# Kernel tuning notes

Hardware: AMD Instinct MI355X
Metric: run time of the kernel (lower is better)

The kernel has to match this reference:

```python
import jax, jax.numpy as jnp
import numpy as np

B, S, D, H, KD, HID = 8, 1024, 512, 8, 64, 32


def setup_inputs() -> dict:
    key = jax.random.key(0)
    ks = jax.random.split(key, 13)
    s = 0.05
    return {
        "src": jax.random.normal(ks[0], (B, S, D), jnp.float32),
        "Wq": jax.random.normal(ks[1], (H, KD, D), jnp.float32) * s,
        "Wk": jax.random.normal(ks[2], (H, KD, D), jnp.float32) * s,
        "Wv": jax.random.normal(ks[3], (H, KD, D), jnp.float32) * s,
        "c_raw": jnp.ones((H,), jnp.float32),              # nn.Parameter(1.0) per head
        "L": jnp.full((H,), 2.0, jnp.float32),             # nn.Parameter(2.0) per head
        "w1": jax.random.normal(ks[4], (H, HID), jnp.float32) * s,   # Linear(1,HID) weight
        "b1": jax.random.normal(ks[5], (H, HID), jnp.float32) * s,
        "W2": jax.random.normal(ks[6], (H, HID, HID), jnp.float32) * s,  # [out,in]
        "b2": jax.random.normal(ks[7], (H, HID), jnp.float32) * s,
        "w3": jax.random.normal(ks[8], (H, HID), jnp.float32) * s,   # Linear(HID,1) weight
        "b3": jax.random.normal(ks[9], (H,), jnp.float32) * s,
        "Wo": jax.random.normal(ks[10], (D, D), jnp.float32) * s,
    }


def _gelu(x):
    return jax.nn.gelu(x, approximate=False)  # torch nn.GELU default (erf)


def reference(src, Wq, Wk, Wv, c_raw, L, w1, b1, W2, b2, w3, b3, Wo):
    Bc, Sc, Dc = src.shape
    Hh, Kd = Wq.shape[0], Wq.shape[1]
    # ---- FIRE bias: raw[i,j] = log1p(c*(i-j)) / log1p(c*max(L, i+1)) for j<i else 0
    ii = jnp.arange(Sc, dtype=jnp.float32)[:, None]   # [S,1]
    jj = jnp.arange(Sc, dtype=jnp.float32)[None, :]   # [1,S]
    d = ii - jj                                       # [S,S]
    c = jax.nn.softplus(c_raw)[:, None, None]         # [H,1,1]
    num = jnp.log1p(c * jnp.where(d > 0, d, 1.0)[None])          # safe for d<=0
    den = jnp.log1p(c * jnp.maximum(L[:, None, None], ii[None] + 1.0))
    raw = jnp.where(d[None] > 0, num / den, 0.0)      # [H,S,S]
    # ---- f_theta MLP applied elementwise (Linear(1,h)->GELU->Linear(h,h)->GELU->Linear(h,1))
    h1 = _gelu(raw[..., None] * w1[:, None, None, :] + b1[:, None, None, :])   # [H,S,S,HID]
    h2 = _gelu(jnp.einsum('hijk,hlk->hijl', h1, W2) + b2[:, None, None, :])    # [H,S,S,HID]
    bias = jnp.einsum('hijk,hk->hij', h2, w3) + b3[:, None, None]              # [H,S,S]
    # ---- causal mask (strict upper triangle -> -inf)
    causal = jnp.arange(Sc)[None, :] > jnp.arange(Sc)[:, None]
    bias = jnp.where(causal[None], -jnp.inf, bias)
    # ---- attention per head
    q = jnp.einsum('bsd,hkd->bhsk', src, Wq)
    k = jnp.einsum('bsd,hkd->bhsk', src, Wk)
    v = jnp.einsum('bsd,hkd->bhsk', src, Wv)
    logits = jnp.einsum('bhik,bhjk->bhij', q, k) / jnp.sqrt(jnp.float32(Kd)) + bias[None]
    attn = jax.nn.softmax(logits, axis=-1)
    o = jnp.einsum('bhij,bhjk->bhik', attn, v)        # [B,H,S,KD]
    o = jnp.transpose(o, (0, 2, 1, 3)).reshape(Bc, Sc, Hh * Kd)  # concat heads
    return o @ Wo.T
```

## Files before the change

kernel.cpp:

```cpp
#include <hip/hip_runtime.h>
#include <math.h>

#define S_LEN 1024
#define NHEAD 8
#define BATCH 8
#define KDIM  64
#define HID   32
#define NT    2048
#define TRI(q) ((q) * ((q) + 1) / 2)
#define PERM(m) (((m) & 0x20) | (((m) & 0x0C) << 1) | (((m) & 0x10) >> 2) | ((m) & 3))
#define SWZ(row) (((((row) >> 3) & 1) << 2) | ((row) & 3))

typedef __attribute__((ext_vector_type(8))) short bf16x8;
typedef __attribute__((ext_vector_type(4))) float f32x4;
typedef unsigned short ushort_t;

__device__ inline ushort_t f2bf(float f) {
  union { float f; unsigned u; } v; v.f = f;
  unsigned u = v.u;
  return (ushort_t)((u + 0x7FFFu + ((u >> 16) & 1u)) >> 16);
}
__device__ inline float bf2f(ushort_t u) {
  union { unsigned x; float f; } v; v.x = ((unsigned)u) << 16; return v.f;
}

__device__ inline void gl_lds16(const ushort_t* g, ushort_t* l) {
  __builtin_amdgcn_global_load_lds(
      (const __attribute__((address_space(1))) unsigned int*)g,
      (__attribute__((address_space(3))) unsigned int*)l, 16, 0, 0);
}

__global__ __launch_bounds__(256) void prep(
    const float* __restrict__ s, const float* __restrict__ wq,
    const float* __restrict__ wk, const float* __restrict__ wv,
    const float* __restrict__ wo,
    ushort_t* __restrict__ sb, ushort_t* __restrict__ wqb,
    ushort_t* __restrict__ wkb, ushort_t* __restrict__ wvb,
    ushort_t* __restrict__ wob,
    const float* __restrict__ c_raw, const float* __restrict__ Lp,
    const float* __restrict__ w1, const float* __restrict__ b1,
    const float* __restrict__ W2, const float* __restrict__ b2,
    const float* __restrict__ w3, const float* __restrict__ b3,
    float* __restrict__ num_g, float* __restrict__ rden_g,
    float* __restrict__ gtab_g) {
  __shared__ float h1s[8][33];
  const int bx = blockIdx.x;
  const int tid = threadIdx.x;
  if (bx < 5120) {
    const float* src; ushort_t* dst; int base; float scale = 1.0f;
    if (bx < 4096)      { src = s;  dst = sb;  base = bx; }
    else if (bx < 4352) { src = wq; dst = wqb; base = bx - 4096; scale = 0.125f; }
    else if (bx < 4608) { src = wk; dst = wkb; base = bx - 4352; }
    else if (bx < 4864) { src = wv; dst = wvb; base = bx - 4608; }
    else                { src = wo; dst = wob; base = bx - 4864; }
    const int i = (base * 256 + tid) * 4;
    float4 v = *(const float4*)&src[i];
    ushort4 o;
    o.x = f2bf(v.x * scale); o.y = f2bf(v.y * scale);
    o.z = f2bf(v.z * scale); o.w = f2bf(v.w * scale);
    *(ushort4*)&dst[i] = o;
  } else {
    const int idx = bx - 5120;
    const int h = idx / 257;
    const int xb = idx % 257;
    const float cr = c_raw[h];
    const float c = (cr > 20.f) ? cr : log1pf(expf(cr));
    const int gid = xb * 256 + tid;
    if (gid < S_LEN) {
      num_g[h * S_LEN + gid] = log1pf(c * (float)gid);
      rden_g[h * S_LEN + gid] = 1.0f / log1pf(c * fmaxf(Lp[h], (float)(gid + 1)));
    }
    const int pl = tid >> 5;
    const int j = tid & 31;
    const int pt = xb * 8 + pl;
    const float x = (float)pt * (1.0f / NT);
    float v = x * w1[h * HID + j] + b1[h * HID + j];
    h1s[pl][j] = 0.5f * v * (1.0f + erff(v * 0.70710678118f));
    __syncthreads();
    float sm = b2[h * HID + j];
    const float* w2r = W2 + ((size_t)(h * HID + j)) * HID;
    #pragma unroll
    for (int k = 0; k < HID; ++k) sm += w2r[k] * h1s[pl][k];
    float g = 0.5f * sm * (1.0f + erff(sm * 0.70710678118f));
    float y = w3[h * HID + j] * g;
    #pragma unroll
    for (int off = 1; off < 32; off <<= 1) y += __shfl_xor(y, off);
    if (j == 0 && pt <= NT) gtab_g[h * (NT + 1) + pt] = y + b3[h];
  }
}

__device__ __forceinline__ void gemm_tile(
    ushort_t* sAB, const ushort_t* __restrict__ A, const ushort_t* __restrict__ Wp,
    void* __restrict__ outp, int mode, int m0, int n0, int tid) {
  ushort_t* sA = sAB;
  ushort_t* sB = sAB + 8192;
  const int lane = tid & 63, w = tid >> 6, quad = lane >> 4, l16 = lane & 15;
  const int wr = w >> 1, wc = w & 1;
  f32x4 acc[4][4];
  #pragma unroll
  for (int ia = 0; ia < 4; ++ia)
    #pragma unroll
    for (int ib = 0; ib < 4; ++ib) acc[ia][ib] = (f32x4)0.0f;

  const int r8 = lane >> 3;
  const int gc = (lane & 7) ^ r8;
  const int sw = l16 & 7;

  for (int kt = 0; kt < 512; kt += 64) {
    __syncthreads();
    #pragma unroll
    for (int j = 0; j < 4; ++j) {
      const int row = j * 32 + w * 8 + r8;
      gl_lds16(&A[(size_t)(m0 + row) * 512 + kt + gc * 8], &sA[(j * 32 + w * 8) * 64]);
      gl_lds16(&Wp[(size_t)(n0 + row) * 512 + kt + gc * 8], &sB[(j * 32 + w * 8) * 64]);
    }
    __syncthreads();
    #pragma unroll
    for (int ks = 0; ks < 2; ++ks) {
      const int off = ((ks * 4 + quad) ^ sw) * 8;
      bf16x8 af[4], bfr[4];
      #pragma unroll
      for (int i = 0; i < 4; ++i) {
        af[i] = *(bf16x8*)&sA[(wr * 64 + i * 16 + l16) * 64 + off];
        bfr[i] = *(bf16x8*)&sB[(wc * 64 + i * 16 + l16) * 64 + off];
      }
      #pragma unroll
      for (int ia = 0; ia < 4; ++ia)
        #pragma unroll
        for (int ib = 0; ib < 4; ++ib)
          acc[ia][ib] = __builtin_amdgcn_mfma_f32_16x16x32_bf16(af[ia], bfr[ib], acc[ia][ib], 0, 0, 0);
    }
  }

  if (mode == 2) {
    __syncthreads();
    #pragma unroll
    for (int ia = 0; ia < 4; ++ia)
      #pragma unroll
      for (int ib = 0; ib < 4; ++ib)
        #pragma unroll
        for (int r = 0; r < 4; ++r) {
          int nl = wc * 64 + ib * 16 + l16;
          int ml = wr * 64 + ia * 16 + quad * 4 + r;
          sAB[nl * 128 + (((ml >> 3) ^ (nl & 7)) * 8) + (ml & 7)] = f2bf(acc[ia][ib][r]);
        }
    __syncthreads();
    const int nl = tid >> 1, halfm = tid & 1;
    const int ng = n0 + nl, hh = ng >> 6, kd = ng & 63;
    const int bb = m0 >> 10, sbase = m0 & 1023;
    ushort_t* vout = (ushort_t*)outp + (((size_t)(bb * NHEAD + hh)) * KDIM + kd) * S_LEN;
    #pragma unroll
    for (int c2 = 0; c2 < 8; ++c2) {
      int mc = halfm * 8 + c2;
      bf16x8 vr = *(bf16x8*)&sAB[nl * 128 + ((mc ^ (nl & 7)) * 8)];
      *(bf16x8*)&vout[sbase + mc * 8] = vr;
    }
    return;
  }
  #pragma unroll
  for (int ia = 0; ia < 4; ++ia) {
    #pragma unroll
    for (int ib = 0; ib < 4; ++ib) {
      #pragma unroll
      for (int r = 0; r < 4; ++r) {
        int m = m0 + wr * 64 + ia * 16 + quad * 4 + r;
        int n = n0 + wc * 64 + ib * 16 + l16;
        float v = acc[ia][ib][r];
        if (mode == 1) {
          int bb = m >> 10, ss = m & 1023, hh = n >> 6, kd = n & 63;
          ((ushort_t*)outp)[(((size_t)(bb * NHEAD + hh)) * S_LEN + ss) * KDIM + kd] = f2bf(v);
        } else {
          ((float*)outp)[(size_t)m * 512 + n] = v;
        }
      }
    }
  }
}

__global__ __launch_bounds__(256) void gemm_bias(
    const ushort_t* __restrict__ A,
    const ushort_t* __restrict__ W0, const ushort_t* __restrict__ W1,
    const ushort_t* __restrict__ W2w,
    void* __restrict__ out0, void* __restrict__ out1, void* __restrict__ out2,
    int scatter, int nGemm,
    const float* __restrict__ num_g, const float* __restrict__ rden_g,
    const float* __restrict__ gtab_g, ushort_t* __restrict__ biaspre) {
  __shared__ __align__(16) ushort_t sAB[16384];
  const int tid = threadIdx.x;
  if ((int)blockIdx.x < nGemm) {
    const int z = blockIdx.x >> 8;
    const int idx = blockIdx.x & 255;
    const int m0 = (idx & 63) * 128;
    const int n0 = (idx >> 6) * 128;
    const ushort_t* Wp = (z == 0) ? W0 : (z == 1) ? W1 : W2w;
    void* outp = (z == 0) ? out0 : (z == 1) ? out1 : out2;
    const int mode = scatter ? ((z == 2) ? 2 : 1) : 0;
    gemm_tile(sAB, A, Wp, outp, mode, m0, n0, tid);
  } else {
    const int idx = blockIdx.x - nGemm;
    const int h = idx / 68;
    const int pair = idx % 68;
    float* gtab_s = (float*)sAB;
    float* num_s = gtab_s + 2052;
    float* rden_s = num_s + 1024;
    for (int i = tid; i <= NT; i += 256) gtab_s[i] = gtab_g[h * (NT + 1) + i];
    for (int i = tid; i < S_LEN; i += 256) num_s[i] = num_g[h * S_LEN + i];
    const int sub = tid >> 7, tid2 = tid & 127;
    const int tileIdx = pair * 2 + sub;
    int qt = 0;
    while (TRI(qt + 1) <= tileIdx) ++qt;
    const int t = tileIdx - TRI(qt);
    if (tid2 < 64) rden_s[sub * 64 + tid2] = rden_g[h * S_LEN + qt * 64 + tid2];
    __syncthreads();
    const int w = tid2 >> 6, lane = tid2 & 63, quad = lane >> 4, l16 = lane & 15;
    ushort_t vals[32];
    #pragma unroll
    for (int qg = 0; qg < 2; ++qg) {
      const int iloc = w * 32 + qg * 16 + l16;
      const int i = qt * 64 + iloc;
      const float rden = rden_s[sub * 64 + iloc];
      #pragma unroll
      for (int nb = 0; nb < 4; ++nb)
        #pragma unroll
        for (int r = 0; r < 4; ++r) {
          const int m = nb * 16 + quad * 4 + r;
          const int j = t * 64 + PERM(m);
          ushort_t out;
          if (j > i) {
            out = 0xFF80;
          } else {
            const int d = i - j;
            float x = num_s[d] * rden;
            float tf = x * (float)NT;
            int it = (int)tf; it = it < (NT - 1) ? it : (NT - 1);
            float fr = tf - (float)it;
            float ga = gtab_s[it];
            out = f2bf(ga + (gtab_s[it + 1] - ga) * fr);
          }
          vals[qg * 16 + nb * 4 + r] = out;
        }
    }
    ushort_t* dst = &biaspre[((size_t)(h * 136 + tileIdx) * 128 + tid2) * 32];
    uint4 u[2];
    #pragma unroll
    for (int half = 0; half < 2; ++half) {
      #pragma unroll
      for (int v = 0; v < 8; ++v) ((ushort_t*)&u[0])[v] = vals[half * 16 + v];
      #pragma unroll
      for (int v = 0; v < 8; ++v) ((ushort_t*)&u[1])[v] = vals[half * 16 + 8 + v];
      *(uint4*)(dst + half * 16) = u[0];
      *(uint4*)(dst + half * 16 + 8) = u[1];
    }
  }
}

__global__ __launch_bounds__(128) void fire_attn_mfma(
    const ushort_t* __restrict__ Qg, const ushort_t* __restrict__ Kg,
    const ushort_t* __restrict__ Vtg, const ushort_t* __restrict__ biaspre,
    ushort_t* __restrict__ Ob) {
  __shared__ __align__(16) ushort_t Ks[64 * 64];
  __shared__ __align__(16) ushort_t Vt[64 * 64];
  const int tid = threadIdx.x;
  const int lane = tid & 63, w = tid >> 6, quad = lane >> 4, l16 = lane & 15;
  const int g = blockIdx.x >> 6;
  const int qt = (g < 8) ? (15 - g) : (g - 8);
  const int bh = blockIdx.x & 63, h = bh & 7, b = bh >> 3;

  bf16x8 q[2][2];
  {
    const size_t qb = (size_t)bh * S_LEN + qt * 64 + w * 32;
    #pragma unroll
    for (int qg = 0; qg < 2; ++qg)
      #pragma unroll
      for (int ks = 0; ks < 2; ++ks)
        q[qg][ks] = *(const bf16x8*)&Qg[(qb + qg * 16 + l16) * KDIM + ks * 32 + quad * 8];
  }

  const size_t kb = (size_t)bh * S_LEN * KDIM;
  const ushort_t* bptr = &biaspre[((size_t)(h * 136 + TRI(qt)) * 128 + tid) * 32];
  const int srow8 = lane >> 3;
  const int sc = lane & 7;

  f32x4 o[2][4];
  float ll[2] = {0.f, 0.f};
  #pragma unroll
  for (int qg = 0; qg < 2; ++qg)
    #pragma unroll
    for (int nb = 0; nb < 4; ++nb) o[qg][nb] = (f32x4)0.0f;

  for (int t = 0; t <= qt; ++t) {
    __syncthreads();
    #pragma unroll
    for (int j = 0; j < 4; ++j) {
      const int row = (w * 4 + j) * 8 + srow8;
      const int cc = sc ^ SWZ(row);
      gl_lds16(&Kg[kb + (size_t)(t * 64 + row) * 64 + cc * 8], &Ks[(w * 4 + j) * 512]);
      gl_lds16(&Vtg[kb + (size_t)row * 1024 + t * 64 + cc * 8], &Vt[(w * 4 + j) * 512]);
    }
    __syncthreads();

    uint4 bb0 = ((const uint4*)(bptr + (size_t)t * 4096))[0];
    uint4 bb1 = ((const uint4*)(bptr + (size_t)t * 4096))[1];
    uint4 bb2 = ((const uint4*)(bptr + (size_t)t * 4096))[2];
    uint4 bb3 = ((const uint4*)(bptr + (size_t)t * 4096))[3];

    f32x4 s[2][4];
    #pragma unroll
    for (int qg = 0; qg < 2; ++qg)
      #pragma unroll
      for (int nb = 0; nb < 4; ++nb) s[qg][nb] = (f32x4)0.0f;
    #pragma unroll
    for (int ks = 0; ks < 2; ++ks) {
      #pragma unroll
      for (int nb = 0; nb < 4; ++nb) {
        const int rk = PERM(nb * 16 + l16);
        bf16x8 ak = *(bf16x8*)&Ks[rk * 64 + (((ks * 4 + quad) ^ SWZ(rk)) * 8)];
        #pragma unroll
        for (int qg = 0; qg < 2; ++qg)
          s[qg][nb] = __builtin_amdgcn_mfma_f32_16x16x32_bf16(ak, q[qg][ks], s[qg][nb], 0, 0, 0);
      }
    }

    ushort_t eb[2][16];
    #pragma unroll
    for (int qg = 0; qg < 2; ++qg) {
      #pragma unroll
      for (int nb = 0; nb < 4; ++nb)
        #pragma unroll
        for (int r = 0; r < 4; ++r) {
          const int v = qg * 16 + nb * 4 + r;
          const uint4& bq = (v < 8) ? bb0 : (v < 16) ? bb1 : (v < 24) ? bb2 : bb3;
          ushort_t bu = ((const ushort_t*)&bq)[v & 7];
          float p = __expf(s[qg][nb][r] + bf2f(bu));
          ll[qg] += p;
          eb[qg][nb * 4 + r] = f2bf(p);
        }
    }

    #pragma unroll
    for (int ks = 0; ks < 2; ++ks) {
      bf16x8 pf[2];
      #pragma unroll
      for (int qg = 0; qg < 2; ++qg) {
        union { bf16x8 v; unsigned u[4]; } pk;
        pk.u[0] = (unsigned)eb[qg][(2 * ks) * 4 + 0] | ((unsigned)eb[qg][(2 * ks) * 4 + 1] << 16);
        pk.u[1] = (unsigned)eb[qg][(2 * ks) * 4 + 2] | ((unsigned)eb[qg][(2 * ks) * 4 + 3] << 16);
        pk.u[2] = (unsigned)eb[qg][(2 * ks + 1) * 4 + 0] | ((unsigned)eb[qg][(2 * ks + 1) * 4 + 1] << 16);
        pk.u[3] = (unsigned)eb[qg][(2 * ks + 1) * 4 + 2] | ((unsigned)eb[qg][(2 * ks + 1) * 4 + 3] << 16);
        pf[qg] = pk.v;
      }
      #pragma unroll
      for (int nb = 0; nb < 4; ++nb) {
        const int rv = nb * 16 + l16;
        bf16x8 av = *(bf16x8*)&Vt[rv * 64 + (((ks * 4 + quad) ^ SWZ(rv)) * 8)];
        #pragma unroll
        for (int qg = 0; qg < 2; ++qg)
          o[qg][nb] = __builtin_amdgcn_mfma_f32_16x16x32_bf16(av, pf[qg], o[qg][nb], 0, 0, 0);
      }
    }
  }

  #pragma unroll
  for (int qg = 0; qg < 2; ++qg) {
    float rs = ll[qg];
    rs += __shfl_xor(rs, 16);
    rs += __shfl_xor(rs, 32);
    const float rl = 1.0f / rs;
    const size_t ob = ((size_t)(b * S_LEN + qt * 64 + w * 32 + qg * 16 + l16)) * 512 + h * KDIM;
    #pragma unroll
    for (int nb = 0; nb < 4; ++nb) {
      ushort4 ov;
      ov.x = f2bf(o[qg][nb][0] * rl);
      ov.y = f2bf(o[qg][nb][1] * rl);
      ov.z = f2bf(o[qg][nb][2] * rl);
      ov.w = f2bf(o[qg][nb][3] * rl);
      *(ushort4*)&Ob[ob + nb * 16 + quad * 4] = ov;
    }
  }
}

extern "C" void kernel_launch(void* const* d_in, const int* in_sizes, int n_in,
                              void* d_out, int out_size, void* d_ws, size_t ws_size,
                              hipStream_t stream) {
  const float* src   = (const float*)d_in[0];
  const float* Wq    = (const float*)d_in[1];
  const float* Wk    = (const float*)d_in[2];
  const float* Wv    = (const float*)d_in[3];
  const float* c_raw = (const float*)d_in[4];
  const float* Lp    = (const float*)d_in[5];
  const float* w1    = (const float*)d_in[6];
  const float* b1    = (const float*)d_in[7];
  const float* W2    = (const float*)d_in[8];
  const float* b2    = (const float*)d_in[9];
  const float* w3    = (const float*)d_in[10];
  const float* b3    = (const float*)d_in[11];
  const float* Wo    = (const float*)d_in[12];
  float* outp = (float*)d_out;

  const size_t SRC_E = 4194304;
  const size_t W_E   = 262144;
  const size_t QKV_E = 4194304;
  ushort_t* srcb = (ushort_t*)d_ws;
  ushort_t* Wqb  = srcb + SRC_E;
  ushort_t* Wkb  = Wqb + W_E;
  ushort_t* Wvb  = Wkb + W_E;
  ushort_t* Wob  = Wvb + W_E;
  ushort_t* Qb   = Wob + W_E;
  ushort_t* Kb   = Qb + QKV_E;
  ushort_t* Vtb  = Kb + QKV_E;
  ushort_t* Obb  = Vtb + QKV_E;
  ushort_t* biaspre = Obb + QKV_E;
  float* numb  = (float*)(biaspre + (size_t)NHEAD * 136 * 128 * 32);
  float* rdenb = numb + NHEAD * S_LEN;
  float* gtabb = rdenb + NHEAD * S_LEN;

  hipLaunchKernelGGL(prep, dim3(7176), dim3(256), 0, stream,
                     src, Wq, Wk, Wv, Wo, srcb, Wqb, Wkb, Wvb, Wob,
                     c_raw, Lp, w1, b1, W2, b2, w3, b3, numb, rdenb, gtabb);
  hipLaunchKernelGGL(gemm_bias, dim3(1312), dim3(256), 0, stream,
                     srcb, Wqb, Wkb, Wvb, (void*)Qb, (void*)Kb, (void*)Vtb,
                     1, 768, numb, rdenb, gtabb, biaspre);
  hipLaunchKernelGGL(fire_attn_mfma, dim3(1024), dim3(128), 0, stream,
                     Qb, Kb, Vtb, biaspre, Obb);
  hipLaunchKernelGGL(gemm_bias, dim3(256), dim3(256), 0, stream,
                     Obb, Wob, Wob, Wob, (void*)outp, (void*)outp, (void*)outp,
                     0, 256, numb, rdenb, gtabb, biaspre);
}
```

Measured before the change: 170.9 us.

## Register-prefetch next K/V and GEMM tiles instead of direct global-to-LDS loads

Replaces the global_load_lds direct-to-LDS copies in both the projection GEMM and the attention loop with register-staged loads. The next tile is fetched into registers while the current tile is being computed, then written to swizzled LDS at the start of the next iteration. This is meant to hide global memory latency behind MFMA work. The cost is extra VGPRs and a separate LDS store pass, which could lower occupancy.

```diff
diff --git a/kernel.cpp b/kernel.cpp
--- a/kernel.cpp
+++ b/kernel.cpp
@@ -22,12 +22,6 @@
 }
 __device__ inline float bf2f(ushort_t u) {
   union { unsigned x; float f; } v; v.x = ((unsigned)u) << 16; return v.f;
-}
-
-__device__ inline void gl_lds16(const ushort_t* g, ushort_t* l) {
-  __builtin_amdgcn_global_load_lds(
-      (const __attribute__((address_space(1))) unsigned int*)g,
-      (__attribute__((address_space(3))) unsigned int*)l, 16, 0, 0);
 }
 
 __global__ __launch_bounds__(256) void prep(
@@ -102,19 +96,34 @@
     #pragma unroll
     for (int ib = 0; ib < 4; ++ib) acc[ia][ib] = (f32x4)0.0f;
 
-  const int r8 = lane >> 3;
-  const int gc = (lane & 7) ^ r8;
   const int sw = l16 & 7;
 
-  for (int kt = 0; kt < 512; kt += 64) {
-    __syncthreads();
-    #pragma unroll
-    for (int j = 0; j < 4; ++j) {
-      const int row = j * 32 + w * 8 + r8;
-      gl_lds16(&A[(size_t)(m0 + row) * 512 + kt + gc * 8], &sA[(j * 32 + w * 8) * 64]);
-      gl_lds16(&Wp[(size_t)(n0 + row) * 512 + kt + gc * 8], &sB[(j * 32 + w * 8) * 64]);
-    }
-    __syncthreads();
+  const int row = tid >> 1, half = tid & 1, r7 = row & 7;
+  const ushort_t* ag = &A[(size_t)(m0 + row) * 512 + half * 32];
+  const ushort_t* bg = &Wp[(size_t)(n0 + row) * 512 + half * 32];
+  uint4 pa[4], pb[4];
+  #pragma unroll
+  for (int i = 0; i < 4; ++i) {
+    pa[i] = *(const uint4*)(ag + i * 8);
+    pb[i] = *(const uint4*)(bg + i * 8);
+  }
+
+  for (int kt8 = 0; kt8 < 8; ++kt8) {
+    __syncthreads();
+    #pragma unroll
+    for (int i = 0; i < 4; ++i) {
+      const int c = half * 4 + i;
+      *(uint4*)&sA[row * 64 + ((c ^ r7) * 8)] = pa[i];
+      *(uint4*)&sB[row * 64 + ((c ^ r7) * 8)] = pb[i];
+    }
+    __syncthreads();
+    if (kt8 < 7) {
+      #pragma unroll
+      for (int i = 0; i < 4; ++i) {
+        pa[i] = *(const uint4*)(ag + (kt8 + 1) * 64 + i * 8);
+        pb[i] = *(const uint4*)(bg + (kt8 + 1) * 64 + i * 8);
+      }
+    }
     #pragma unroll
     for (int ks = 0; ks < 2; ++ks) {
       const int off = ((ks * 4 + quad) ^ sw) * 8;
@@ -278,8 +287,17 @@
 
   const size_t kb = (size_t)bh * S_LEN * KDIM;
   const ushort_t* bptr = &biaspre[((size_t)(h * 136 + TRI(qt)) * 128 + tid) * 32];
-  const int srow8 = lane >> 3;
-  const int sc = lane & 7;
+
+  const int srow = tid >> 1, shalf = tid & 1;
+  const int sswz = SWZ(srow);
+  const ushort_t* kg = &Kg[kb + (size_t)srow * 64 + shalf * 32];
+  const ushort_t* vg = &Vtg[kb + (size_t)srow * 1024 + shalf * 32];
+  uint4 pk[4], pv[4];
+  #pragma unroll
+  for (int i = 0; i < 4; ++i) {
+    pk[i] = *(const uint4*)(kg + i * 8);
+    pv[i] = *(const uint4*)(vg + i * 8);
+  }
 
   f32x4 o[2][4];
   float ll[2] = {0.f, 0.f};
@@ -291,13 +309,19 @@
   for (int t = 0; t <= qt; ++t) {
     __syncthreads();
     #pragma unroll
-    for (int j = 0; j < 4; ++j) {
-      const int row = (w * 4 + j) * 8 + srow8;
-      const int cc = sc ^ SWZ(row);
-      gl_lds16(&Kg[kb + (size_t)(t * 64 + row) * 64 + cc * 8], &Ks[(w * 4 + j) * 512]);
-      gl_lds16(&Vtg[kb + (size_t)row * 1024 + t * 64 + cc * 8], &Vt[(w * 4 + j) * 512]);
-    }
-    __syncthreads();
+    for (int i = 0; i < 4; ++i) {
+      const int c = shalf * 4 + i;
+      *(uint4*)&Ks[srow * 64 + ((c ^ sswz) * 8)] = pk[i];
+      *(uint4*)&Vt[srow * 64 + ((c ^ sswz) * 8)] = pv[i];
+    }
+    __syncthreads();
+    if (t < qt) {
+      #pragma unroll
+      for (int i = 0; i < 4; ++i) {
+        pk[i] = *(const uint4*)(kg + (size_t)(t + 1) * 4096 + i * 8);
+        pv[i] = *(const uint4*)(vg + (size_t)(t + 1) * 64 + i * 8);
+      }
+    }
 
     uint4 bb0 = ((const uint4*)(bptr + (size_t)t * 4096))[0];
     uint4 bb1 = ((const uint4*)(bptr + (size_t)t * 4096))[1];
@@ -342,12 +366,12 @@
       bf16x8 pf[2];
       #pragma unroll
       for (int qg = 0; qg < 2; ++qg) {
-        union { bf16x8 v; unsigned u[4]; } pk;
-        pk.u[0] = (unsigned)eb[qg][(2 * ks) * 4 + 0] | ((unsigned)eb[qg][(2 * ks) * 4 + 1] << 16);
-        pk.u[1] = (unsigned)eb[qg][(2 * ks) * 4 + 2] | ((unsigned)eb[qg][(2 * ks) * 4 + 3] << 16);
-        pk.u[2] = (unsigned)eb[qg][(2 * ks + 1) * 4 + 0] | ((unsigned)eb[qg][(2 * ks + 1) * 4 + 1] << 16);
-        pk.u[3] = (unsigned)eb[qg][(2 * ks + 1) * 4 + 2] | ((unsigned)eb[qg][(2 * ks + 1) * 4 + 3] << 16);
-        pf[qg] = pk.v;
+        union { bf16x8 v; unsigned u[4]; } pkx;
+        pkx.u[0] = (unsigned)eb[qg][(2 * ks) * 4 + 0] | ((unsigned)eb[qg][(2 * ks) * 4 + 1] << 16);
+        pkx.u[1] = (unsigned)eb[qg][(2 * ks) * 4 + 2] | ((unsigned)eb[qg][(2 * ks) * 4 + 3] << 16);
+        pkx.u[2] = (unsigned)eb[qg][(2 * ks + 1) * 4 + 0] | ((unsigned)eb[qg][(2 * ks + 1) * 4 + 1] << 16);
+        pkx.u[3] = (unsigned)eb[qg][(2 * ks + 1) * 4 + 2] | ((unsigned)eb[qg][(2 * ks + 1) * 4 + 3] << 16);
+        pf[qg] = pkx.v;
       }
       #pragma unroll
       for (int nb = 0; nb < 4; ++nb) {
```

After: 257.3 us. 1.51x slower.
